# Kernel optimization log

Hardware: AMD Instinct MI355X
Metric: run time of the kernel (lower is better)

The kernel has to match this reference:

```python
import jax, jax.numpy as jnp
import numpy as np

D_MODEL = 1024
N_HEADS = 16
HEAD_DIM = D_MODEL // N_HEADS
MAX_POS = 4096
ROPE_BASE = 10000.0
NEG_INF = -1e30


def _rope_cache(max_pos, head_dim, base):
    inv_freq = 1.0 / (base ** (np.arange(0, head_dim, 2, dtype=np.float32) / head_dim))
    t = np.arange(max_pos, dtype=np.float32)[:, None] * inv_freq[None, :]  # [P, D/2]
    cos = np.repeat(np.cos(t), 2, axis=-1)  # [P, D] (repeat_interleave)
    sin = np.repeat(np.sin(t), 2, axis=-1)
    return jnp.asarray(cos), jnp.asarray(sin)

COS_CACHE, SIN_CACHE = _rope_cache(MAX_POS, HEAD_DIM, ROPE_BASE)


def _rotate_half(x):
    # interleaved pairs: (x0,x1,x2,x3,...) -> (-x1,x0,-x3,x2,...)
    x1 = x[..., ::2]
    x2 = x[..., 1::2]
    return jnp.stack((-x2, x1), axis=-1).reshape(x.shape)


def setup_inputs() -> dict:
    key = jax.random.key(0)
    k0, k1, k2 = jax.random.split(key, 3)
    B, S = 4, 1024
    hidden_states = jax.random.normal(k0, (B, S, D_MODEL), dtype=jnp.float32)
    positions = jnp.arange(S, dtype=jnp.int64 if jax.config.jax_enable_x64 else jnp.int32)
    causal_mask = jnp.triu(jnp.ones((S, S), dtype=bool), k=1)  # True above diagonal -> masked
    # learned params (torch nn.Linear weight layout: [out, in], y = x @ W.T)
    Wqkv = jax.random.normal(k1, (3 * D_MODEL, D_MODEL), dtype=jnp.float32) * (D_MODEL ** -0.5)
    Wout = jax.random.normal(k2, (D_MODEL, D_MODEL), dtype=jnp.float32) * (D_MODEL ** -0.5)
    return {"hidden_states": hidden_states, "positions": positions,
            "causal_mask": causal_mask, "Wqkv": Wqkv, "Wout": Wout}


def reference(hidden_states, positions, causal_mask, Wqkv, Wout):
    B, S, D = hidden_states.shape
    qkv = hidden_states @ Wqkv.T                                   # [B,S,3D]
    qkv = qkv.reshape(B, S, 3, N_HEADS, HEAD_DIM)
    qkv = jnp.transpose(qkv, (2, 0, 3, 1, 4))                      # [3,B,H,S,Dh]
    q, k, v = qkv[0], qkv[1], qkv[2]
    # RoPE
    pos = jnp.clip(positions, 0, MAX_POS - 1)
    if pos.ndim == 1:
        pos = pos[None, :]
    cos = COS_CACHE[pos][:, None, :, :].astype(q.dtype)            # [B,1,S,Dh]
    sin = SIN_CACHE[pos][:, None, :, :].astype(q.dtype)
    q = q * cos + _rotate_half(q) * sin
    k = k * cos + _rotate_half(k) * sin
    # SDPA with causal bias (F.scaled_dot_product_attention default scaling)
    scale = HEAD_DIM ** -0.5
    scores = jnp.einsum('bhqd,bhkd->bhqk', q, k) * scale           # [B,H,S,S]
    scores = jnp.where(causal_mask[None, None, :, :], NEG_INF, scores)
    probs = jax.nn.softmax(scores, axis=-1)
    attn = jnp.einsum('bhqk,bhkd->bhqd', probs, v)                 # [B,H,S,Dh]
    attn = jnp.transpose(attn, (0, 2, 1, 3)).reshape(B, S, D)
    return attn @ Wout.T
```

## Files before the change

kernel.cpp:

```cpp
#include <hip/hip_runtime.h>

typedef __attribute__((ext_vector_type(8))) short short8;
typedef __attribute__((ext_vector_type(4))) float f32x4;

#define MFMA(a, b, c) __builtin_amdgcn_mfma_f32_16x16x32_bf16((a), (b), (c), 0, 0, 0)

#define S_LEN 1024
#define DM 1024
#define NHEADS 16
#define HD 64
#define NBH 64
#define MAXPOS 4096

__device__ __forceinline__ ushort f2bf(float f) {
    unsigned u = __builtin_bit_cast(unsigned, f);
    u += 0x7fffu + ((u >> 16) & 1u);
    return (ushort)(u >> 16);
}
__device__ __forceinline__ float bf2f(ushort h) {
    return __builtin_bit_cast(float, (unsigned)h << 16);
}

__device__ __forceinline__ void gload16(const ushort* g, ushort* l) {
    __builtin_amdgcn_global_load_lds(
        (const __attribute__((address_space(1))) unsigned int*)g,
        (__attribute__((address_space(3))) unsigned int*)l, 16, 0, 0);
}

__global__ __launch_bounds__(256) void k_build_tab(float* __restrict__ tab) {
    int id = blockIdx.x * 256 + threadIdx.x;
    int p = id >> 5, i = id & 31;
    float inv = powf(10000.f, -(float)(2 * i) / 64.f);
    float t = (float)p * inv;
    float s, c;
    sincosf(t, &s, &c);
    tab[2 * id] = c;
    tab[2 * id + 1] = s;
}

__global__ __launch_bounds__(256) void k_cvt3(const float4* __restrict__ hs,
                                              const float4* __restrict__ wqkv,
                                              const float4* __restrict__ wout,
                                              ushort4* __restrict__ hsB,
                                              ushort4* __restrict__ wqkvB,
                                              ushort4* __restrict__ woutB) {
    int id = blockIdx.x * 256 + threadIdx.x;
    const float4* src;
    ushort4* dst;
    int off;
    if (id < 1048576)      { src = hs;   dst = hsB;   off = id; }
    else if (id < 1835008) { src = wqkv; dst = wqkvB; off = id - 1048576; }
    else                   { src = wout; dst = woutB; off = id - 1835008; }
    float4 v = src[off];
    ushort4 o;
    o.x = f2bf(v.x); o.y = f2bf(v.y); o.z = f2bf(v.z); o.w = f2bf(v.w);
    dst[off] = o;
}

template <int MODE>
__global__ __launch_bounds__(256, 3) void k_gemm(
    const ushort* __restrict__ A, const ushort* __restrict__ BT,
    float* __restrict__ Cf,
    const int* __restrict__ pos, const float* __restrict__ tab,
    ushort* __restrict__ Qh, ushort* __restrict__ Kh, ushort* __restrict__ Vt,
    int M, int N, int K, int nbx) {
    __shared__ __align__(16) ushort SH[3 * 8192];
    const int tid = threadIdx.x;
    const int lane = tid & 63, wave = tid >> 6;
    const int wr = wave >> 1, wc = wave & 1;
    const int l15 = lane & 15, lhi = lane >> 4;
    const int nby = gridDim.x / nbx;
    const int xcd = blockIdx.x & 7, idx = blockIdx.x >> 3;
    const int Creg = nbx >> 1, Rreg = nby >> 2;
    const int by = (xcd >> 1) * Rreg + idx / Creg;
    const int bx = (xcd & 1) * Creg + idx % Creg;
    const int m0 = by << 7, n0 = bx << 7;

    const int srow = tid >> 2;
    const int scol = (((tid >> 2) & 3) ^ ((tid >> 4) & 3) ^ (tid & 3)) << 3;
    const int fcol = ((lhi ^ ((l15 & 3) ^ ((l15 >> 2) & 3)))) << 3;

    f32x4 acc[4][4];
#pragma unroll
    for (int i = 0; i < 4; ++i)
#pragma unroll
        for (int j = 0; j < 4; ++j) acc[i][j] = 0;

#define STAGE(bs, kb)                                                           \
    do {                                                                        \
        ushort* bb = SH + (bs) * 8192;                                          \
        gload16(&A[(size_t)(m0 + srow) * K + (kb) + scol], bb + tid * 8);       \
        gload16(&A[(size_t)(m0 + 64 + srow) * K + (kb) + scol],                 \
                bb + 2048 + tid * 8);                                           \
        gload16(&BT[(size_t)(n0 + srow) * K + (kb) + scol],                     \
                bb + 4096 + tid * 8);                                           \
        gload16(&BT[(size_t)(n0 + 64 + srow) * K + (kb) + scol],                \
                bb + 6144 + tid * 8);                                           \
    } while (0)

    const int nk = K >> 5;
    STAGE(0, 0);
    STAGE(1, 32);
    int bi = 0;
    for (int t = 0; t < nk; ++t) {
        if (t + 1 < nk) {
            asm volatile("s_waitcnt vmcnt(4)" ::: "memory");
        } else {
            asm volatile("s_waitcnt vmcnt(0)" ::: "memory");
        }
        __builtin_amdgcn_s_barrier();
        __builtin_amdgcn_sched_barrier(0);
        if (t + 2 < nk) {
            int bs = bi + 2;
            if (bs >= 3) bs -= 3;
            STAGE(bs, (t + 2) << 5);
        }
        const ushort* bufA = SH + bi * 8192;
        const ushort* bufB = bufA + 4096;
        short8 a[4], b[4];
#pragma unroll
        for (int fm = 0; fm < 4; ++fm)
            a[fm] = *(const short8*)&bufA[(wr * 64 + fm * 16 + l15) * 32 + fcol];
#pragma unroll
        for (int fn = 0; fn < 4; ++fn)
            b[fn] = *(const short8*)&bufB[(wc * 64 + fn * 16 + l15) * 32 + fcol];
#pragma unroll
        for (int fm = 0; fm < 4; ++fm)
#pragma unroll
            for (int fn = 0; fn < 4; ++fn)
                acc[fm][fn] = MFMA(a[fm], b[fn], acc[fm][fn]);
        bi = (bi == 2) ? 0 : bi + 1;
    }
#undef STAGE
    __syncthreads();

    if (MODE == 0) {
#pragma unroll
        for (int fm = 0; fm < 4; ++fm)
#pragma unroll
            for (int fn = 0; fn < 4; ++fn)
#pragma unroll
                for (int i = 0; i < 4; ++i) {
                    int row = m0 + wr * 64 + fm * 16 + lhi * 4 + i;
                    int col = n0 + wc * 64 + fn * 16 + l15;
                    Cf[(size_t)row * N + col] = acc[fm][fn][i];
                }
    } else {
        const int sec = n0 >> 10;
        if (sec < 2) {
            ushort* dstb = sec == 0 ? Qh : Kh;
            const float qs = sec == 0 ? 0.125f : 1.0f;
#pragma unroll
            for (int fm = 0; fm < 4; ++fm)
#pragma unroll
                for (int i = 0; i < 4; ++i) {
                    const int row = m0 + wr * 64 + fm * 16 + lhi * 4 + i;
                    const int b = row >> 10, s = row & 1023;
                    int p = pos[s];
                    p = p < 0 ? 0 : (p > MAXPOS - 1 ? MAXPOS - 1 : p);
#pragma unroll
                    for (int fn = 0; fn < 4; ++fn) {
                        const int col = n0 + wc * 64 + fn * 16 + l15;
                        const int cw = col & 1023;
                        const int h = cw >> 6, d = cw & 63;
                        const float c  = tab[((size_t)p * 32 + (d >> 1)) * 2];
                        const float sn = tab[((size_t)p * 32 + (d >> 1)) * 2 + 1];
                        const float v = acc[fm][fn][i];
                        const float pr = __shfl_xor(v, 1);
                        const float o = (d & 1) ? (v * c + pr * sn) : (v * c - pr * sn);
                        dstb[((size_t)((b * 16 + h) * 1024 + s)) * 64 + d] = f2bf(o * qs);
                    }
                }
        } else {
            ushort (*T)[132] = (ushort(*)[132]) & SH[0];
#pragma unroll
            for (int fm = 0; fm < 4; ++fm)
#pragma unroll
                for (int fn = 0; fn < 4; ++fn)
#pragma unroll
                    for (int i = 0; i < 4; ++i)
                        T[wr * 64 + fm * 16 + lhi * 4 + i][wc * 64 + fn * 16 + l15] =
                            f2bf(acc[fm][fn][i]);
            __syncthreads();
            const int b = m0 >> 10, s0 = m0 & 1023;
            const int dd = tid & 127, scg = tid >> 7;
            const int hv = ((n0 & 1023) >> 6) + (dd >> 6);
            const int d = dd & 63;
            ushort* dst = Vt + ((size_t)(b * 16 + hv) * 64 + d) * S_LEN + s0;
#pragma unroll
            for (int j = 0; j < 8; ++j) {
                const int ch = scg * 8 + j;
                __align__(16) ushort tmp[8];
#pragma unroll
                for (int e = 0; e < 8; ++e) tmp[e] = T[ch * 8 + e][dd];
                *(uint4*)&dst[ch * 8] = *(uint4*)tmp;
            }
        }
    }
}

__global__ __launch_bounds__(256, 3) void k_attn(const ushort* __restrict__ Qh,
                                                 const ushort* __restrict__ Kh,
                                                 const ushort* __restrict__ Vt,
                                                 ushort* __restrict__ attnB) {
    __shared__ __align__(16) ushort Ks[2][64][64];
    __shared__ __align__(16) ushort Vs[2][64][64];
    __shared__ __align__(16) ushort P[4][16][72];
    const int bh = blockIdx.x;
    const int g  = 15 - blockIdx.y;
    const int tid = threadIdx.x;
    const int wave = tid >> 6, lane = tid & 63;
    const int l15 = lane & 15, lhi = lane >> 4;
    const int b = bh >> 4, h = bh & 15;
    const ushort* Qp = Qh + (size_t)bh * S_LEN * 64;
    const ushort* Kp = Kh + (size_t)bh * S_LEN * 64;
    const ushort* Vp = Vt + (size_t)bh * 64 * S_LEN;
    const int qb = (g << 6) + (wave << 4);
    const int qrowb = qb + lhi * 4;

    const int U0 = tid, U1 = tid + 256;
    const int r0 = U0 >> 3, o0 = ((U0 & 7) ^ (r0 & 7)) << 3;
    const int r1 = U1 >> 3, o1 = ((U1 & 7) ^ (r1 & 7)) << 3;
    ushort* KsF = &Ks[0][0][0];
    ushort* VsF = &Vs[0][0][0];

    short8 aQ0 = *(const short8*)&Qp[(size_t)(qb + l15) * 64 + lhi * 8];
    short8 aQ1 = *(const short8*)&Qp[(size_t)(qb + l15) * 64 + 32 + lhi * 8];

    short8 ones;
#pragma unroll
    for (int j = 0; j < 8; ++j) ones[j] = (short)0x3F80;

    f32x4 O0{}, O1{}, O2{}, O3{}, ssum{};

    gload16(&Kp[(size_t)r0 * 64 + o0], KsF + U0 * 8);
    gload16(&Kp[(size_t)r1 * 64 + o1], KsF + U1 * 8);
    gload16(&Vp[(size_t)r0 * S_LEN + o0], VsF + U0 * 8);
    gload16(&Vp[(size_t)r1 * S_LEN + o1], VsF + U1 * 8);
    __syncthreads();

#define LDSK(s, kk) (*(const short8*)(KsF + (cur << 12) + ((((s) << 4) + l15) << 6) + \
                                      ((((kk) * 4 + lhi) ^ (l15 & 7)) << 3)))
#define LDSV(n, kk) (*(const short8*)(VsF + (cur << 12) + ((((n) << 4) + l15) << 6) + \
                                      ((((kk) * 4 + lhi) ^ (l15 & 7)) << 3)))

    int cur = 0;
    for (int kb = 0; kb <= g; ++kb) {
        const int k0 = kb << 6;
        if (kb < g) {
            const int kn = k0 + 64;
            const int bo = (cur ^ 1) << 12;
            gload16(&Kp[(size_t)(kn + r0) * 64 + o0], KsF + bo + U0 * 8);
            gload16(&Kp[(size_t)(kn + r1) * 64 + o1], KsF + bo + U1 * 8);
            gload16(&Vp[(size_t)r0 * S_LEN + kn + o0], VsF + bo + U0 * 8);
            gload16(&Vp[(size_t)r1 * S_LEN + kn + o1], VsF + bo + U1 * 8);
        }

        __builtin_amdgcn_s_setprio(1);
        f32x4 s0{}, s1{}, s2{}, s3{};
        s0 = MFMA(aQ0, LDSK(0, 0), s0); s0 = MFMA(aQ1, LDSK(0, 1), s0);
        s1 = MFMA(aQ0, LDSK(1, 0), s1); s1 = MFMA(aQ1, LDSK(1, 1), s1);
        s2 = MFMA(aQ0, LDSK(2, 0), s2); s2 = MFMA(aQ1, LDSK(2, 1), s2);
        s3 = MFMA(aQ0, LDSK(3, 0), s3); s3 = MFMA(aQ1, LDSK(3, 1), s3);
        __builtin_amdgcn_s_setprio(0);

        if (kb == g) {
#define EXPSTM(SV, SUB)                                                        \
    _Pragma("unroll") for (int i = 0; i < 4; ++i) {                            \
        float v = SV[i];                                                       \
        if (k0 + (SUB) * 16 + l15 > qrowb + i) v = -1e30f;                     \
        P[wave][lhi * 4 + i][(SUB) * 16 + l15] = f2bf(__expf(v - 8.f));        \
    }
            EXPSTM(s0, 0) EXPSTM(s1, 1) EXPSTM(s2, 2) EXPSTM(s3, 3)
#undef EXPSTM
        } else {
#define EXPST(SV, SUB)                                                         \
    _Pragma("unroll") for (int i = 0; i < 4; ++i) {                            \
        P[wave][lhi * 4 + i][(SUB) * 16 + l15] = f2bf(__expf(SV[i] - 8.f));    \
    }
            EXPST(s0, 0) EXPST(s1, 1) EXPST(s2, 2) EXPST(s3, 3)
#undef EXPST
        }

        short8 aP0 = *(const short8*)&P[wave][l15][lhi * 8];
        short8 aP1 = *(const short8*)&P[wave][l15][32 + lhi * 8];
        __builtin_amdgcn_s_setprio(1);
        ssum = MFMA(aP0, ones, ssum); ssum = MFMA(aP1, ones, ssum);
        O0 = MFMA(aP0, LDSV(0, 0), O0); O0 = MFMA(aP1, LDSV(0, 1), O0);
        O1 = MFMA(aP0, LDSV(1, 0), O1); O1 = MFMA(aP1, LDSV(1, 1), O1);
        O2 = MFMA(aP0, LDSV(2, 0), O2); O2 = MFMA(aP1, LDSV(2, 1), O2);
        O3 = MFMA(aP0, LDSV(3, 0), O3); O3 = MFMA(aP1, LDSV(3, 1), O3);
        __builtin_amdgcn_s_setprio(0);

        __syncthreads();
        cur ^= 1;
    }
#undef LDSK
#undef LDSV

    f32x4 inv;
#pragma unroll
    for (int i = 0; i < 4; ++i) inv[i] = 1.f / ssum[i];
#define WOUT(OV, N)                                                            \
    _Pragma("unroll") for (int i = 0; i < 4; ++i) {                            \
        int row = qb + lhi * 4 + i;                                            \
        attnB[((size_t)(b * S_LEN + row)) * DM + h * 64 + (N) * 16 + l15] =    \
            f2bf(OV[i] * inv[i]);                                              \
    }
    WOUT(O0, 0) WOUT(O1, 1) WOUT(O2, 2) WOUT(O3, 3)
#undef WOUT
}

extern "C" void kernel_launch(void* const* d_in, const int* in_sizes, int n_in,
                              void* d_out, int out_size, void* d_ws, size_t ws_size,
                              hipStream_t stream) {
    (void)in_sizes; (void)n_in; (void)out_size; (void)ws_size;
    const float* hs   = (const float*)d_in[0];
    const int*   pos  = (const int*)d_in[1];
    const float* Wqkv = (const float*)d_in[3];
    const float* Wout = (const float*)d_in[4];
    float* out = (float*)d_out;

    char* ws = (char*)d_ws;
    size_t off = 0;
    ushort* hsB   = (ushort*)(ws + off); off += (size_t)4096 * 1024 * 2;
    ushort* WqkvB = (ushort*)(ws + off); off += (size_t)3072 * 1024 * 2;
    ushort* WoutB = (ushort*)(ws + off); off += (size_t)1024 * 1024 * 2;
    ushort* Qh    = (ushort*)(ws + off); off += (size_t)NBH * 1024 * 64 * 2;
    ushort* Kh    = (ushort*)(ws + off); off += (size_t)NBH * 1024 * 64 * 2;
    ushort* Vt    = (ushort*)(ws + off); off += (size_t)NBH * 64 * 1024 * 2;
    ushort* attnB = (ushort*)(ws + off); off += (size_t)4096 * 1024 * 2;
    float*  tab   = (float*)(ws + off);  off += (size_t)4096 * 32 * 2 * 4;

    k_build_tab<<<512, 256, 0, stream>>>(tab);
    k_cvt3<<<8192, 256, 0, stream>>>((const float4*)hs, (const float4*)Wqkv,
                                     (const float4*)Wout, (ushort4*)hsB,
                                     (ushort4*)WqkvB, (ushort4*)WoutB);

    k_gemm<1><<<768, 256, 0, stream>>>(hsB, WqkvB, nullptr, pos, tab,
                                       Qh, Kh, Vt, 4096, 3072, 1024, 24);

    k_attn<<<dim3(64, 16), 256, 0, stream>>>(Qh, Kh, Vt, attnB);

    k_gemm<0><<<256, 256, 0, stream>>>(attnB, WoutB, out, nullptr, nullptr,
                                       nullptr, nullptr, nullptr, 4096, 1024, 1024, 8);
}
```

Baseline: 94.68 us.

## Use 256x256-tile 8-wave GEMM with 4-stage pipeline for QKV projection

Adds a dedicated QKV projection kernel that uses 256x256 output tiles, 512 threads (8 waves each computing 128x64), and a 4-buffer global-to-LDS pipeline with explicit vmcnt waits. It keeps the fused RoPE epilogue for Q/K and the transposed V writeback, now done in two halves through LDS. The goal is more data reuse per loaded byte and better latency hiding than the 128x128 tile version. The cost is that only 192 blocks are launched for 256 CUs, which leaves many CUs idle, and register pressure is higher. The old MODE 1 path and a sync after the main loop are removed from the generic GEMM.

```diff
diff --git a/kernel.cpp b/kernel.cpp
--- a/kernel.cpp
+++ b/kernel.cpp
@@ -55,6 +55,133 @@
     ushort4 o;
     o.x = f2bf(v.x); o.y = f2bf(v.y); o.z = f2bf(v.z); o.w = f2bf(v.w);
     dst[off] = o;
+}
+
+__global__ __launch_bounds__(512, 2) void k_gemm256(
+    const ushort* __restrict__ A, const ushort* __restrict__ BT,
+    const int* __restrict__ pos, const float* __restrict__ tab,
+    ushort* __restrict__ Qh, ushort* __restrict__ Kh, ushort* __restrict__ Vt) {
+    __shared__ __align__(16) ushort SH[4 * 16384];
+    const int K = 1024;
+    const int tid = threadIdx.x;
+    const int lane = tid & 63, wave = tid >> 6;
+    const int wr = wave >> 2, wc = wave & 3;
+    const int l15 = lane & 15, lhi = lane >> 4;
+    const int bx = blockIdx.x % 12, by = blockIdx.x / 12;
+    const int m0 = by << 8, n0 = bx << 8;
+    const int fcol = ((lhi ^ ((l15 & 3) ^ ((l15 >> 2) & 3)))) << 3;
+
+    f32x4 acc[8][4];
+#pragma unroll
+    for (int i = 0; i < 8; ++i)
+#pragma unroll
+        for (int j = 0; j < 4; ++j) acc[i][j] = 0;
+
+#define STAGE(bs, kb)                                                           \
+    do {                                                                        \
+        ushort* bb = SH + (bs) * 16384;                                         \
+        _Pragma("unroll") for (int k = 0; k < 4; ++k) {                         \
+            const int u = tid + k * 512;                                        \
+            const int r = (u & 1023) >> 2;                                      \
+            const int sc = ((u & 3) ^ (r & 3) ^ ((r >> 2) & 3)) << 3;           \
+            const ushort* src = (k < 2)                                         \
+                ? &A[(size_t)(m0 + r) * K + (kb) + sc]                          \
+                : &BT[(size_t)(n0 + r) * K + (kb) + sc];                        \
+            gload16(src, bb + u * 8);                                           \
+        }                                                                       \
+    } while (0)
+
+    const int nk = K >> 5;
+    STAGE(0, 0);
+    STAGE(1, 32);
+    STAGE(2, 64);
+    int bi = 0;
+    for (int t = 0; t < nk; ++t) {
+        if (t + 2 < nk) {
+            asm volatile("s_waitcnt vmcnt(8)" ::: "memory");
+        } else if (t + 1 < nk) {
+            asm volatile("s_waitcnt vmcnt(4)" ::: "memory");
+        } else {
+            asm volatile("s_waitcnt vmcnt(0)" ::: "memory");
+        }
+        __builtin_amdgcn_s_barrier();
+        __builtin_amdgcn_sched_barrier(0);
+        if (t + 3 < nk) STAGE((bi + 3) & 3, (t + 3) << 5);
+        const ushort* buf = SH + bi * 16384;
+        short8 afr[8], bfr[4];
+#pragma unroll
+        for (int nf = 0; nf < 4; ++nf)
+            bfr[nf] = *(const short8*)&buf[8192 + (wc * 64 + nf * 16 + l15) * 32 + fcol];
+#pragma unroll
+        for (int mf = 0; mf < 8; ++mf)
+            afr[mf] = *(const short8*)&buf[(wr * 128 + mf * 16 + l15) * 32 + fcol];
+#pragma unroll
+        for (int mf = 0; mf < 8; ++mf)
+#pragma unroll
+            for (int nf = 0; nf < 4; ++nf)
+                acc[mf][nf] = MFMA(afr[mf], bfr[nf], acc[mf][nf]);
+        bi = (bi + 1) & 3;
+    }
+#undef STAGE
+    __syncthreads();
+
+    const int sec = n0 >> 10;
+    if (sec < 2) {
+        ushort* dstb = sec == 0 ? Qh : Kh;
+        const float qs = sec == 0 ? 0.125f : 1.0f;
+#pragma unroll
+        for (int mf = 0; mf < 8; ++mf)
+#pragma unroll
+            for (int i = 0; i < 4; ++i) {
+                const int row = m0 + wr * 128 + mf * 16 + lhi * 4 + i;
+                const int b = row >> 10, s = row & 1023;
+                int p = pos[s];
+                p = p < 0 ? 0 : (p > MAXPOS - 1 ? MAXPOS - 1 : p);
+#pragma unroll
+                for (int nf = 0; nf < 4; ++nf) {
+                    const int col = n0 + wc * 64 + nf * 16 + l15;
+                    const int cw = col & 1023;
+                    const int h = cw >> 6, d = cw & 63;
+                    const float c  = tab[((size_t)p * 32 + (d >> 1)) * 2];
+                    const float sn = tab[((size_t)p * 32 + (d >> 1)) * 2 + 1];
+                    const float v = acc[mf][nf][i];
+                    const float pr = __shfl_xor(v, 1);
+                    const float o = (d & 1) ? (v * c + pr * sn) : (v * c - pr * sn);
+                    dstb[((size_t)((b * 16 + h) * 1024 + s)) * 64 + d] = f2bf(o * qs);
+                }
+            }
+    } else {
+        ushort (*T)[264] = (ushort(*)[264]) & SH[0];
+        const int bb = m0 >> 10;
+        const int dd = tid & 255, sg = tid >> 8;
+        const int hv = ((n0 & 1023) >> 6) + (dd >> 6);
+        const int d = dd & 63;
+#pragma unroll
+        for (int h = 0; h < 2; ++h) {
+            if (wr == h) {
+#pragma unroll
+                for (int mf = 0; mf < 8; ++mf)
+#pragma unroll
+                    for (int nf = 0; nf < 4; ++nf)
+#pragma unroll
+                        for (int i = 0; i < 4; ++i)
+                            T[mf * 16 + lhi * 4 + i][wc * 64 + nf * 16 + l15] =
+                                f2bf(acc[mf][nf][i]);
+            }
+            __syncthreads();
+            const int s0 = (m0 & 1023) + h * 128;
+            ushort* dst = Vt + ((size_t)(bb * 16 + hv) * 64 + d) * S_LEN + s0;
+#pragma unroll
+            for (int j = 0; j < 8; ++j) {
+                const int ch = sg * 8 + j;
+                __align__(16) ushort tmp[8];
+#pragma unroll
+                for (int e = 0; e < 8; ++e) tmp[e] = T[ch * 8 + e][dd];
+                *(uint4*)&dst[ch * 8] = *(uint4*)tmp;
+            }
+            __syncthreads();
+        }
+    }
 }
 
 template <int MODE>
@@ -132,7 +259,6 @@
         bi = (bi == 2) ? 0 : bi + 1;
     }
 #undef STAGE
-    __syncthreads();
 
     if (MODE == 0) {
 #pragma unroll
@@ -145,57 +271,6 @@
                     int col = n0 + wc * 64 + fn * 16 + l15;
                     Cf[(size_t)row * N + col] = acc[fm][fn][i];
                 }
-    } else {
-        const int sec = n0 >> 10;
-        if (sec < 2) {
-            ushort* dstb = sec == 0 ? Qh : Kh;
-            const float qs = sec == 0 ? 0.125f : 1.0f;
-#pragma unroll
-            for (int fm = 0; fm < 4; ++fm)
-#pragma unroll
-                for (int i = 0; i < 4; ++i) {
-                    const int row = m0 + wr * 64 + fm * 16 + lhi * 4 + i;
-                    const int b = row >> 10, s = row & 1023;
-                    int p = pos[s];
-                    p = p < 0 ? 0 : (p > MAXPOS - 1 ? MAXPOS - 1 : p);
-#pragma unroll
-                    for (int fn = 0; fn < 4; ++fn) {
-                        const int col = n0 + wc * 64 + fn * 16 + l15;
-                        const int cw = col & 1023;
-                        const int h = cw >> 6, d = cw & 63;
-                        const float c  = tab[((size_t)p * 32 + (d >> 1)) * 2];
-                        const float sn = tab[((size_t)p * 32 + (d >> 1)) * 2 + 1];
-                        const float v = acc[fm][fn][i];
-                        const float pr = __shfl_xor(v, 1);
-                        const float o = (d & 1) ? (v * c + pr * sn) : (v * c - pr * sn);
-                        dstb[((size_t)((b * 16 + h) * 1024 + s)) * 64 + d] = f2bf(o * qs);
-                    }
-                }
-        } else {
-            ushort (*T)[132] = (ushort(*)[132]) & SH[0];
-#pragma unroll
-            for (int fm = 0; fm < 4; ++fm)
-#pragma unroll
-                for (int fn = 0; fn < 4; ++fn)
-#pragma unroll
-                    for (int i = 0; i < 4; ++i)
-                        T[wr * 64 + fm * 16 + lhi * 4 + i][wc * 64 + fn * 16 + l15] =
-                            f2bf(acc[fm][fn][i]);
-            __syncthreads();
-            const int b = m0 >> 10, s0 = m0 & 1023;
-            const int dd = tid & 127, scg = tid >> 7;
-            const int hv = ((n0 & 1023) >> 6) + (dd >> 6);
-            const int d = dd & 63;
-            ushort* dst = Vt + ((size_t)(b * 16 + hv) * 64 + d) * S_LEN + s0;
-#pragma unroll
-            for (int j = 0; j < 8; ++j) {
-                const int ch = scg * 8 + j;
-                __align__(16) ushort tmp[8];
-#pragma unroll
-                for (int e = 0; e < 8; ++e) tmp[e] = T[ch * 8 + e][dd];
-                *(uint4*)&dst[ch * 8] = *(uint4*)tmp;
-            }
-        }
     }
 }
 
@@ -337,8 +412,7 @@
                                      (const float4*)Wout, (ushort4*)hsB,
                                      (ushort4*)WqkvB, (ushort4*)WoutB);
 
-    k_gemm<1><<<768, 256, 0, stream>>>(hsB, WqkvB, nullptr, pos, tab,
-                                       Qh, Kh, Vt, 4096, 3072, 1024, 24);
+    k_gemm256<<<192, 512, 0, stream>>>(hsB, WqkvB, pos, tab, Qh, Kh, Vt);
 
     k_attn<<<dim3(64, 16), 256, 0, stream>>>(Qh, Kh, Vt, attnB);
 
```

New measurement: 97.67 us. +3.2%, slower.

## Pair causal query blocks per attention workgroup and fold RoPE table into convert kernel

Applied to the files above, without the earlier changes.

Each attention workgroup now handles two query tiles, g and 15-g. They share the same K/V tiles streamed from LDS, so every block does the same total work (17 key blocks) and the causal triangle is balanced across blocks. The grid is halved to 512 blocks. Separately, the RoPE cos/sin table build is merged into the bf16 conversion kernel, which removes one launch. The cost is twice the accumulator registers per wave and fewer blocks to spread across CUs.

```diff
diff --git a/kernel.cpp b/kernel.cpp
--- a/kernel.cpp
+++ b/kernel.cpp
@@ -27,34 +27,35 @@
         (__attribute__((address_space(3))) unsigned int*)l, 16, 0, 0);
 }
 
-__global__ __launch_bounds__(256) void k_build_tab(float* __restrict__ tab) {
-    int id = blockIdx.x * 256 + threadIdx.x;
-    int p = id >> 5, i = id & 31;
-    float inv = powf(10000.f, -(float)(2 * i) / 64.f);
-    float t = (float)p * inv;
-    float s, c;
-    sincosf(t, &s, &c);
-    tab[2 * id] = c;
-    tab[2 * id + 1] = s;
-}
-
 __global__ __launch_bounds__(256) void k_cvt3(const float4* __restrict__ hs,
                                               const float4* __restrict__ wqkv,
                                               const float4* __restrict__ wout,
                                               ushort4* __restrict__ hsB,
                                               ushort4* __restrict__ wqkvB,
-                                              ushort4* __restrict__ woutB) {
+                                              ushort4* __restrict__ woutB,
+                                              float* __restrict__ tab) {
     int id = blockIdx.x * 256 + threadIdx.x;
-    const float4* src;
-    ushort4* dst;
-    int off;
-    if (id < 1048576)      { src = hs;   dst = hsB;   off = id; }
-    else if (id < 1835008) { src = wqkv; dst = wqkvB; off = id - 1048576; }
-    else                   { src = wout; dst = woutB; off = id - 1835008; }
-    float4 v = src[off];
-    ushort4 o;
-    o.x = f2bf(v.x); o.y = f2bf(v.y); o.z = f2bf(v.z); o.w = f2bf(v.w);
-    dst[off] = o;
+    if (id < 2097152) {
+        const float4* src;
+        ushort4* dst;
+        int off;
+        if (id < 1048576)      { src = hs;   dst = hsB;   off = id; }
+        else if (id < 1835008) { src = wqkv; dst = wqkvB; off = id - 1048576; }
+        else                   { src = wout; dst = woutB; off = id - 1835008; }
+        float4 v = src[off];
+        ushort4 o;
+        o.x = f2bf(v.x); o.y = f2bf(v.y); o.z = f2bf(v.z); o.w = f2bf(v.w);
+        dst[off] = o;
+    } else {
+        int t = id - 2097152;
+        int p = t >> 5, i = t & 31;
+        float inv = powf(10000.f, -(float)(2 * i) / 64.f);
+        float th = (float)p * inv;
+        float s, c;
+        sincosf(th, &s, &c);
+        tab[2 * t] = c;
+        tab[2 * t + 1] = s;
+    }
 }
 
 template <int MODE>
@@ -207,7 +208,9 @@
     __shared__ __align__(16) ushort Vs[2][64][64];
     __shared__ __align__(16) ushort P[4][16][72];
     const int bh = blockIdx.x;
-    const int g  = 15 - blockIdx.y;
+    const int g  = blockIdx.y;
+    const int gA = g, gB = 15 - g;
+    const int nkb = gB + 1;
     const int tid = threadIdx.x;
     const int wave = tid >> 6, lane = tid & 63;
     const int l15 = lane & 15, lhi = lane >> 4;
@@ -215,8 +218,10 @@
     const ushort* Qp = Qh + (size_t)bh * S_LEN * 64;
     const ushort* Kp = Kh + (size_t)bh * S_LEN * 64;
     const ushort* Vp = Vt + (size_t)bh * 64 * S_LEN;
-    const int qb = (g << 6) + (wave << 4);
-    const int qrowb = qb + lhi * 4;
+    const int qbA = (gA << 6) + (wave << 4);
+    const int qbB = (gB << 6) + (wave << 4);
+    const int qrowbA = qbA + lhi * 4;
+    const int qrowbB = qbB + lhi * 4;
 
     const int U0 = tid, U1 = tid + 256;
     const int r0 = U0 >> 3, o0 = ((U0 & 7) ^ (r0 & 7)) << 3;
@@ -224,14 +229,17 @@
     ushort* KsF = &Ks[0][0][0];
     ushort* VsF = &Vs[0][0][0];
 
-    short8 aQ0 = *(const short8*)&Qp[(size_t)(qb + l15) * 64 + lhi * 8];
-    short8 aQ1 = *(const short8*)&Qp[(size_t)(qb + l15) * 64 + 32 + lhi * 8];
+    short8 aQA0 = *(const short8*)&Qp[(size_t)(qbA + l15) * 64 + lhi * 8];
+    short8 aQA1 = *(const short8*)&Qp[(size_t)(qbA + l15) * 64 + 32 + lhi * 8];
+    short8 aQB0 = *(const short8*)&Qp[(size_t)(qbB + l15) * 64 + lhi * 8];
+    short8 aQB1 = *(const short8*)&Qp[(size_t)(qbB + l15) * 64 + 32 + lhi * 8];
 
     short8 ones;
 #pragma unroll
     for (int j = 0; j < 8; ++j) ones[j] = (short)0x3F80;
 
-    f32x4 O0{}, O1{}, O2{}, O3{}, ssum{};
+    f32x4 OA0{}, OA1{}, OA2{}, OA3{}, ssumA{};
+    f32x4 OB0{}, OB1{}, OB2{}, OB3{}, ssumB{};
 
     gload16(&Kp[(size_t)r0 * 64 + o0], KsF + U0 * 8);
     gload16(&Kp[(size_t)r1 * 64 + o1], KsF + U1 * 8);
@@ -243,11 +251,21 @@
                                       ((((kk) * 4 + lhi) ^ (l15 & 7)) << 3)))
 #define LDSV(n, kk) (*(const short8*)(VsF + (cur << 12) + ((((n) << 4) + l15) << 6) + \
                                       ((((kk) * 4 + lhi) ^ (l15 & 7)) << 3)))
+#define EXPST(SV, SUB)                                                         \
+    _Pragma("unroll") for (int i = 0; i < 4; ++i) {                            \
+        P[wave][lhi * 4 + i][(SUB) * 16 + l15] = f2bf(__expf(SV[i] - 8.f));    \
+    }
+#define EXPSTM(SV, SUB, QROWB)                                                 \
+    _Pragma("unroll") for (int i = 0; i < 4; ++i) {                            \
+        float v = SV[i];                                                       \
+        if (k0 + (SUB) * 16 + l15 > (QROWB) + i) v = -1e30f;                   \
+        P[wave][lhi * 4 + i][(SUB) * 16 + l15] = f2bf(__expf(v - 8.f));        \
+    }
 
     int cur = 0;
-    for (int kb = 0; kb <= g; ++kb) {
+    for (int kb = 0; kb < nkb; ++kb) {
         const int k0 = kb << 6;
-        if (kb < g) {
+        if (kb + 1 < nkb) {
             const int kn = k0 + 64;
             const int bo = (cur ^ 1) << 12;
             gload16(&Kp[(size_t)(kn + r0) * 64 + o0], KsF + bo + U0 * 8);
@@ -256,58 +274,82 @@
             gload16(&Vp[(size_t)r1 * S_LEN + kn + o1], VsF + bo + U1 * 8);
         }
 
-        __builtin_amdgcn_s_setprio(1);
-        f32x4 s0{}, s1{}, s2{}, s3{};
-        s0 = MFMA(aQ0, LDSK(0, 0), s0); s0 = MFMA(aQ1, LDSK(0, 1), s0);
-        s1 = MFMA(aQ0, LDSK(1, 0), s1); s1 = MFMA(aQ1, LDSK(1, 1), s1);
-        s2 = MFMA(aQ0, LDSK(2, 0), s2); s2 = MFMA(aQ1, LDSK(2, 1), s2);
-        s3 = MFMA(aQ0, LDSK(3, 0), s3); s3 = MFMA(aQ1, LDSK(3, 1), s3);
-        __builtin_amdgcn_s_setprio(0);
-
-        if (kb == g) {
-#define EXPSTM(SV, SUB)                                                        \
-    _Pragma("unroll") for (int i = 0; i < 4; ++i) {                            \
-        float v = SV[i];                                                       \
-        if (k0 + (SUB) * 16 + l15 > qrowb + i) v = -1e30f;                     \
-        P[wave][lhi * 4 + i][(SUB) * 16 + l15] = f2bf(__expf(v - 8.f));        \
-    }
-            EXPSTM(s0, 0) EXPSTM(s1, 1) EXPSTM(s2, 2) EXPSTM(s3, 3)
-#undef EXPSTM
-        } else {
-#define EXPST(SV, SUB)                                                         \
-    _Pragma("unroll") for (int i = 0; i < 4; ++i) {                            \
-        P[wave][lhi * 4 + i][(SUB) * 16 + l15] = f2bf(__expf(SV[i] - 8.f));    \
-    }
-            EXPST(s0, 0) EXPST(s1, 1) EXPST(s2, 2) EXPST(s3, 3)
-#undef EXPST
-        }
-
-        short8 aP0 = *(const short8*)&P[wave][l15][lhi * 8];
-        short8 aP1 = *(const short8*)&P[wave][l15][32 + lhi * 8];
-        __builtin_amdgcn_s_setprio(1);
-        ssum = MFMA(aP0, ones, ssum); ssum = MFMA(aP1, ones, ssum);
-        O0 = MFMA(aP0, LDSV(0, 0), O0); O0 = MFMA(aP1, LDSV(0, 1), O0);
-        O1 = MFMA(aP0, LDSV(1, 0), O1); O1 = MFMA(aP1, LDSV(1, 1), O1);
-        O2 = MFMA(aP0, LDSV(2, 0), O2); O2 = MFMA(aP1, LDSV(2, 1), O2);
-        O3 = MFMA(aP0, LDSV(3, 0), O3); O3 = MFMA(aP1, LDSV(3, 1), O3);
-        __builtin_amdgcn_s_setprio(0);
+        if (kb <= gA) {
+            __builtin_amdgcn_s_setprio(1);
+            f32x4 s0{}, s1{}, s2{}, s3{};
+            s0 = MFMA(aQA0, LDSK(0, 0), s0); s0 = MFMA(aQA1, LDSK(0, 1), s0);
+            s1 = MFMA(aQA0, LDSK(1, 0), s1); s1 = MFMA(aQA1, LDSK(1, 1), s1);
+            s2 = MFMA(aQA0, LDSK(2, 0), s2); s2 = MFMA(aQA1, LDSK(2, 1), s2);
+            s3 = MFMA(aQA0, LDSK(3, 0), s3); s3 = MFMA(aQA1, LDSK(3, 1), s3);
+            __builtin_amdgcn_s_setprio(0);
+            if (kb == gA) {
+                EXPSTM(s0, 0, qrowbA) EXPSTM(s1, 1, qrowbA)
+                EXPSTM(s2, 2, qrowbA) EXPSTM(s3, 3, qrowbA)
+            } else {
+                EXPST(s0, 0) EXPST(s1, 1) EXPST(s2, 2) EXPST(s3, 3)
+            }
+            short8 aP0 = *(const short8*)&P[wave][l15][lhi * 8];
+            short8 aP1 = *(const short8*)&P[wave][l15][32 + lhi * 8];
+            __builtin_amdgcn_s_setprio(1);
+            ssumA = MFMA(aP0, ones, ssumA); ssumA = MFMA(aP1, ones, ssumA);
+            OA0 = MFMA(aP0, LDSV(0, 0), OA0); OA0 = MFMA(aP1, LDSV(0, 1), OA0);
+            OA1 = MFMA(aP0, LDSV(1, 0), OA1); OA1 = MFMA(aP1, LDSV(1, 1), OA1);
+            OA2 = MFMA(aP0, LDSV(2, 0), OA2); OA2 = MFMA(aP1, LDSV(2, 1), OA2);
+            OA3 = MFMA(aP0, LDSV(3, 0), OA3); OA3 = MFMA(aP1, LDSV(3, 1), OA3);
+            __builtin_amdgcn_s_setprio(0);
+        }
+
+        {
+            __builtin_amdgcn_s_setprio(1);
+            f32x4 s0{}, s1{}, s2{}, s3{};
+            s0 = MFMA(aQB0, LDSK(0, 0), s0); s0 = MFMA(aQB1, LDSK(0, 1), s0);
+            s1 = MFMA(aQB0, LDSK(1, 0), s1); s1 = MFMA(aQB1, LDSK(1, 1), s1);
+            s2 = MFMA(aQB0, LDSK(2, 0), s2); s2 = MFMA(aQB1, LDSK(2, 1), s2);
+            s3 = MFMA(aQB0, LDSK(3, 0), s3); s3 = MFMA(aQB1, LDSK(3, 1), s3);
+            __builtin_amdgcn_s_setprio(0);
+            if (kb == gB) {
+                EXPSTM(s0, 0, qrowbB) EXPSTM(s1, 1, qrowbB)
+                EXPSTM(s2, 2, qrowbB) EXPSTM(s3, 3, qrowbB)
+            } else {
+                EXPST(s0, 0) EXPST(s1, 1) EXPST(s2, 2) EXPST(s3, 3)
+            }
+            short8 aP0 = *(const short8*)&P[wave][l15][lhi * 8];
+            short8 aP1 = *(const short8*)&P[wave][l15][32 + lhi * 8];
+            __builtin_amdgcn_s_setprio(1);
+            ssumB = MFMA(aP0, ones, ssumB); ssumB = MFMA(aP1, ones, ssumB);
+            OB0 = MFMA(aP0, LDSV(0, 0), OB0); OB0 = MFMA(aP1, LDSV(0, 1), OB0);
+            OB1 = MFMA(aP0, LDSV(1, 0), OB1); OB1 = MFMA(aP1, LDSV(1, 1), OB1);
+            OB2 = MFMA(aP0, LDSV(2, 0), OB2); OB2 = MFMA(aP1, LDSV(2, 1), OB2);
+            OB3 = MFMA(aP0, LDSV(3, 0), OB3); OB3 = MFMA(aP1, LDSV(3, 1), OB3);
+            __builtin_amdgcn_s_setprio(0);
+        }
 
         __syncthreads();
         cur ^= 1;
     }
 #undef LDSK
 #undef LDSV
-
-    f32x4 inv;
-#pragma unroll
-    for (int i = 0; i < 4; ++i) inv[i] = 1.f / ssum[i];
-#define WOUT(OV, N)                                                            \
+#undef EXPST
+#undef EXPSTM
+
+#define WOUT(OV, N, QB, INV)                                                   \
     _Pragma("unroll") for (int i = 0; i < 4; ++i) {                            \
-        int row = qb + lhi * 4 + i;                                            \
+        int row = (QB) + lhi * 4 + i;                                          \
         attnB[((size_t)(b * S_LEN + row)) * DM + h * 64 + (N) * 16 + l15] =    \
-            f2bf(OV[i] * inv[i]);                                              \
-    }
-    WOUT(O0, 0) WOUT(O1, 1) WOUT(O2, 2) WOUT(O3, 3)
+            f2bf(OV[i] * INV[i]);                                              \
+    }
+    {
+        f32x4 invA, invB;
+#pragma unroll
+        for (int i = 0; i < 4; ++i) {
+            invA[i] = 1.f / ssumA[i];
+            invB[i] = 1.f / ssumB[i];
+        }
+        WOUT(OA0, 0, qbA, invA) WOUT(OA1, 1, qbA, invA)
+        WOUT(OA2, 2, qbA, invA) WOUT(OA3, 3, qbA, invA)
+        WOUT(OB0, 0, qbB, invB) WOUT(OB1, 1, qbB, invB)
+        WOUT(OB2, 2, qbB, invB) WOUT(OB3, 3, qbB, invB)
+    }
 #undef WOUT
 }
 
@@ -332,15 +374,14 @@
     ushort* attnB = (ushort*)(ws + off); off += (size_t)4096 * 1024 * 2;
     float*  tab   = (float*)(ws + off);  off += (size_t)4096 * 32 * 2 * 4;
 
-    k_build_tab<<<512, 256, 0, stream>>>(tab);
-    k_cvt3<<<8192, 256, 0, stream>>>((const float4*)hs, (const float4*)Wqkv,
+    k_cvt3<<<8704, 256, 0, stream>>>((const float4*)hs, (const float4*)Wqkv,
                                      (const float4*)Wout, (ushort4*)hsB,
-                                     (ushort4*)WqkvB, (ushort4*)WoutB);
+                                     (ushort4*)WqkvB, (ushort4*)WoutB, tab);
 
     k_gemm<1><<<768, 256, 0, stream>>>(hsB, WqkvB, nullptr, pos, tab,
                                        Qh, Kh, Vt, 4096, 3072, 1024, 24);
 
-    k_attn<<<dim3(64, 16), 256, 0, stream>>>(Qh, Kh, Vt, attnB);
+    k_attn<<<dim3(64, 8), 256, 0, stream>>>(Qh, Kh, Vt, attnB);
 
     k_gemm<0><<<256, 256, 0, stream>>>(attnB, WoutB, out, nullptr, nullptr,
                                        nullptr, nullptr, nullptr, 4096, 1024, 1024, 8);
```

Measured after the change: 93.14 us. No clear change (-1.6%).
